# Kernel tuning notes

Hardware: AMD Instinct MI355X
Metric: run time of the kernel (lower is better)

Reference implementation:

```python
import jax, jax.numpy as jnp
import numpy as np

LAYERS = 10
EPS = 1e-08


def setup_inputs() -> dict:
    key = jax.random.key(0)
    # [B, agents, N, N] assignment logits; row 0 along dim 2 is the depot row
    output = jax.random.normal(key, (32, 8, 512, 512), dtype=jnp.float32)
    return {"output": output}


def reference(output):
    # Max-subtraction for numerical stability before exp.
    # Depot row: max over dim 3 only. Other rows: max over dims (1, 3).
    if LAYERS > 0:
        depots_max = jnp.max(output[:, :, :1, :], axis=3, keepdims=True)
        others_max = jnp.max(output[:, :, 1:, :], axis=(1, 3), keepdims=True)
        output = jnp.concatenate(
            [output[:, :, :1, :] - depots_max,
             output[:, :, 1:, :] - others_max],
            axis=2,
        )
    output = jnp.exp(output)
    # Sinkhorn-style alternating normalization; transpose(2,3) each iter
    # alternates which axis gets normalized.
    for _ in range(LAYERS):
        output = jnp.maximum(output, EPS)
        starts = output[:, :, :1, :]
        starts = starts / jnp.sum(starts, axis=3, keepdims=True)
        nexts = output[:, :, 1:, :]
        nexts = nexts / jnp.sum(nexts, axis=(1, 3), keepdims=True)
        output = jnp.concatenate([starts, nexts], axis=2)
        output = jnp.swapaxes(output, 2, 3)
    if LAYERS % 2 != 0:
        output = jnp.swapaxes(output, 2, 3)
    return output
```

## Files before the change

kernel.cpp:

```cpp
#include <hip/hip_runtime.h>
#include <hip/hip_cooperative_groups.h>
#include <math.h>

#define B 32
#define H 8
#define N 512
#define NBLK 256
#define TPB 512
#define RPB 64
#define OFF_E0   8388608
#define OFF_EC   (OFF_E0 + 131072)
#define OFF_PA   (OFF_EC + 131072)
#define OFF_PB   (OFF_PA + 131072)
#define OFF_C0A  (OFF_PB + 131072)
#define OFF_C0B  (OFF_C0A + 2048)

typedef float f32x4 __attribute__((ext_vector_type(4)));

__device__ __forceinline__ float atomLoad(const float* p) {
    return __hip_atomic_load(p, __ATOMIC_RELAXED, __HIP_MEMORY_SCOPE_AGENT);
}
__device__ __forceinline__ float2 atomLoad2(const float* p) {
    unsigned long long u = __hip_atomic_load(
        reinterpret_cast<const unsigned long long*>(p),
        __ATOMIC_RELAXED, __HIP_MEMORY_SCOPE_AGENT);
    union { unsigned long long u; float2 f; } cvt; cvt.u = u;
    return cvt.f;
}
__device__ __forceinline__ void atomStore(float* p, float v) {
    __hip_atomic_store(p, v, __ATOMIC_RELAXED, __HIP_MEMORY_SCOPE_AGENT);
}

__device__ __forceinline__ void group_barrier(int* cnt, int target) {
    __syncthreads();
    if (threadIdx.x == 0) {
        __hip_atomic_fetch_add(cnt, 1, __ATOMIC_RELAXED, __HIP_MEMORY_SCOPE_AGENT);
        while (__hip_atomic_load(cnt, __ATOMIC_RELAXED, __HIP_MEMORY_SCOPE_AGENT) < target)
            __builtin_amdgcn_s_sleep(1);
    }
    __syncthreads();
}

__global__ __launch_bounds__(128) void k_build(const float* __restrict__ in,
                                               float* __restrict__ G,
                                               float* __restrict__ E0,
                                               float* __restrict__ Ec,
                                               int* __restrict__ counters) {
    const int i = blockIdx.x;
    const int b = blockIdx.y;
    const int t = threadIdx.x;
    if (i == 0 && b == 0) {
#pragma unroll
        for (int k = 0; k < 4; ++k) counters[k * 128 + t] = 0;
    }
    const size_t inb = (size_t)b * H * N * N;
    float4 acc = make_float4(0.f, 0.f, 0.f, 0.f);
#pragma unroll
    for (int h = 0; h < H; ++h) {
        const float4 x = *reinterpret_cast<const float4*>(
            in + inb + ((size_t)h * N + i) * N + t * 4);
        float4 e;
        e.x = __expf(x.x); e.y = __expf(x.y); e.z = __expf(x.z); e.w = __expf(x.w);
        acc.x += e.x; acc.y += e.y; acc.z += e.z; acc.w += e.w;
        if (t == 0) Ec[(b * H + h) * N + i] = e.x;
        if (i == 0) *reinterpret_cast<float4*>(E0 + (b * H + h) * N + t * 4) = e;
    }
    *reinterpret_cast<float4*>(G + ((size_t)b * N + i) * N + t * 4) = acc;
}

__global__ __launch_bounds__(TPB) void k_coop(const float* __restrict__ G,
                                              const float* __restrict__ E0,
                                              const float* __restrict__ Ec,
                                              float* __restrict__ partA,
                                              float* __restrict__ partB,
                                              float* __restrict__ c0pA,
                                              float* __restrict__ c0pB,
                                              float* __restrict__ rv,
                                              float* __restrict__ r0v,
                                              float* __restrict__ cv,
                                              float* __restrict__ c0v,
                                              int* __restrict__ counters) {
    __shared__ float Gs[RPB][N];
    __shared__ float E0g[N];
    __shared__ float vec[N];
    __shared__ float EcS[H][RPB];
    __shared__ float rloc[RPB];
    __shared__ float c0rec[H];
    __shared__ float r0loc_s;

    const int blk = blockIdx.x;
    const int b = blk >> 3;
    const int g = blk & 7;
    const int rbase = g * RPB;
    const bool owner = (g == 0);
    const int tid = threadIdx.x;
    const int w = tid >> 6, lane = tid & 63;
    int* cnt = counters + b * 16;

    {
        const float4* Gg = reinterpret_cast<const float4*>(G + ((size_t)(b * N) + rbase) * N);
        float4* Gl = reinterpret_cast<float4*>(&Gs[0][0]);
#pragma unroll
        for (int k = 0; k < RPB * N / 4 / TPB; ++k) {
            const int t = k * TPB + tid;
            __builtin_amdgcn_global_load_lds(
                (const __attribute__((address_space(1))) void*)(Gg + t),
                (__attribute__((address_space(3))) void*)(Gl + t),
                16, 0, 0);
        }
    }
    EcS[tid >> 6][tid & 63] = Ec[(b * H + (tid >> 6)) * N + rbase + (tid & 63)];
    E0g[tid] = E0[(b * H + g) * N + tid];
    const float E00g = Ec[(b * H + g) * N];
    __syncthreads();

    for (int it = 0; it < 5; ++it) {
        if (it == 0) {
            vec[tid] = (tid == 0) ? 0.0f : 1.0f;
            if (tid < H) c0rec[tid] = 1.0f;
        } else {
            const float* pr = (it & 1) ? partB : partA;
            pr += ((size_t)b * N + tid) * 8;
            float cs = 0.0f;
#pragma unroll
            for (int k = 0; k < 4; ++k) {
                float2 d = atomLoad2(pr + 2 * k);
                cs += d.x + d.y;
            }
            vec[tid] = (tid == 0) ? 0.0f : 1.0f / cs;
            if (tid < H) {
                const float* qr = (it & 1) ? c0pB : c0pA;
                qr += (b * 8 + tid) * 8;
                float s = 0.0f;
#pragma unroll
                for (int k = 0; k < 4; ++k) {
                    float2 d = atomLoad2(qr + 2 * k);
                    s += d.x + d.y;
                }
                c0rec[tid] = 1.0f / s;
            }
        }
        __syncthreads();
        float cj[8];
#pragma unroll
        for (int k = 0; k < 8; ++k) cj[k] = vec[lane + 64 * k];
#pragma unroll
        for (int r8 = 0; r8 < 8; ++r8) {
            const int il = w * 8 + r8;
            float pacc = 0.0f;
#pragma unroll
            for (int k = 0; k < 8; ++k) pacc += Gs[il][lane + 64 * k] * cj[k];
#pragma unroll
            for (int s = 32; s > 0; s >>= 1) pacc += __shfl_down(pacc, s, 64);
            if (lane == 0) {
                float s2 = pacc;
#pragma unroll
                for (int h = 0; h < H; ++h) s2 += EcS[h][il] * c0rec[h];
                float rva = 1.0f / s2;
                rloc[il] = rva;
                if (it == 4) rv[b * N + rbase + il] = rva;
            }
        }
        if (w == g) {
            float pacc = 0.0f;
#pragma unroll
            for (int k = 0; k < 8; ++k) pacc += E0g[lane + 64 * k] * cj[k];
#pragma unroll
            for (int s = 32; s > 0; s >>= 1) pacc += __shfl_down(pacc, s, 64);
            if (lane == 0) {
                float v = 1.0f / (pacc + E00g * c0rec[g]);
                r0loc_s = v;
                if (it == 4) r0v[b * H + g] = v;
            }
        }
        __syncthreads();
        {
            float* pw = ((it + 1) & 1) ? partB : partA;
            float* qw = ((it + 1) & 1) ? c0pB : c0pA;
            const float r0l = r0loc_s;
            float acc = 0.0f;
            const int il0 = owner ? 1 : 0;
#pragma unroll 8
            for (int il = il0; il < RPB; ++il) acc += Gs[il][tid] * rloc[il];
            acc += E0g[tid] * r0l;
            atomStore(&pw[((size_t)b * N + tid) * 8 + g], acc);
            float q = EcS[w][lane] * ((owner && lane == 0) ? 0.0f : rloc[lane]);
            if (w == g && lane == 0) q += E00g * r0l;
#pragma unroll
            for (int s = 32; s > 0; s >>= 1) q += __shfl_down(q, s, 64);
            if (lane == 0) atomStore(&qw[(b * 8 + w) * 8 + g], q);
        }
        group_barrier(cnt, (it + 1) * 8);
    }
    if (owner) {
        const float* pr = partB + ((size_t)b * N + tid) * 8;
        float cs = 0.0f;
#pragma unroll
        for (int k = 0; k < 4; ++k) {
            float2 d = atomLoad2(pr + 2 * k);
            cs += d.x + d.y;
        }
        cv[b * N + tid] = (tid == 0) ? 1.0f : 1.0f / cs;
        if (tid < H) {
            const float* qr = c0pB + (b * 8 + tid) * 8;
            float s = 0.0f;
#pragma unroll
            for (int k = 0; k < 4; ++k) {
                float2 d = atomLoad2(qr + 2 * k);
                s += d.x + d.y;
            }
            c0v[b * H + tid] = 1.0f / s;
        }
    }
}

__global__ __launch_bounds__(256) void k_final(const float* __restrict__ in,
                                               const float* __restrict__ rv,
                                               const float* __restrict__ r0v,
                                               const float* __restrict__ cv,
                                               const float* __restrict__ c0v,
                                               float* __restrict__ out) {
    const size_t v0 = (size_t)blockIdx.x * 2048 + threadIdx.x;
    float4 x[8];
#pragma unroll
    for (int s = 0; s < 8; ++s)
        x[s] = reinterpret_cast<const float4*>(in)[v0 + (size_t)s * 256];
#pragma unroll
    for (int s = 0; s < 8; ++s) {
        const size_t v = v0 + (size_t)s * 256;
        const int j4 = (int)(v & 127);
        size_t rest = v >> 7;
        const int i = (int)(rest & 511); rest >>= 9;
        const int h = (int)(rest & 7);
        const int b = (int)(rest >> 3);
        const float R = (i == 0) ? r0v[b * H + h] : rv[b * N + i];
        float4 cl = reinterpret_cast<const float4*>(cv + b * N)[j4];
        if (j4 == 0) cl.x = c0v[b * H + h];
        f32x4 o;
        o.x = __expf(x[s].x) * R * cl.x;
        o.y = __expf(x[s].y) * R * cl.y;
        o.z = __expf(x[s].z) * R * cl.z;
        o.w = __expf(x[s].w) * R * cl.w;
        __builtin_nontemporal_store(o, reinterpret_cast<f32x4*>(out) + v);
    }
}

extern "C" void kernel_launch(void* const* d_in, const int* in_sizes, int n_in,
                              void* d_out, int out_size, void* d_ws, size_t ws_size,
                              hipStream_t stream) {
    (void)in_sizes; (void)n_in; (void)out_size; (void)ws_size;
    const float* in = (const float*)d_in[0];
    float* out = (float*)d_out;
    float* ws = (float*)d_ws;

    float* rv  = ws;
    float* cv  = ws + 16384;
    float* r0v = ws + 32768;
    float* c0v = ws + 33024;
    int* counters = (int*)(ws + 33280);

    float* G   = out;
    float* E0  = out + OFF_E0;
    float* Ec  = out + OFF_EC;
    float* pA  = out + OFF_PA;
    float* pB  = out + OFF_PB;
    float* c0A = out + OFF_C0A;
    float* c0B = out + OFF_C0B;

    k_build<<<dim3(N, B), 128, 0, stream>>>(in, G, E0, Ec, counters);

    void* args[] = {(void*)&G, (void*)&E0, (void*)&Ec, (void*)&pA, (void*)&pB,
                    (void*)&c0A, (void*)&c0B, (void*)&rv, (void*)&r0v,
                    (void*)&cv, (void*)&c0v, (void*)&counters};
    hipLaunchCooperativeKernel(reinterpret_cast<void*>(k_coop), dim3(NBLK), dim3(TPB),
                               args, 0, stream);

    k_final<<<8192, 256, 0, stream>>>(in, rv, r0v, cv, c0v, out);
}
```

Before: 196.4 us.

## Fuse exp/head-sum build stage into cooperative kernel, drop G round-trip

Removes the separate build kernel that computed exp of the input, summed it over heads into a global G matrix, and wrote E0/Ec side arrays. The cooperative kernel now reads the input directly, computes exponentials and head sums in registers, and writes them straight into shared memory. This avoids writing and re-reading the 32 MB G intermediate and one full kernel launch. The cost is that only 256 blocks read the 256 MB input, which may cap memory parallelism, and register pressure rises from the 16 float4 accumulators.

```diff
diff --git a/kernel.cpp b/kernel.cpp
--- a/kernel.cpp
+++ b/kernel.cpp
@@ -8,18 +8,13 @@
 #define NBLK 256
 #define TPB 512
 #define RPB 64
-#define OFF_E0   8388608
-#define OFF_EC   (OFF_E0 + 131072)
-#define OFF_PA   (OFF_EC + 131072)
+#define OFF_PA   8388608
 #define OFF_PB   (OFF_PA + 131072)
 #define OFF_C0A  (OFF_PB + 131072)
 #define OFF_C0B  (OFF_C0A + 2048)
 
 typedef float f32x4 __attribute__((ext_vector_type(4)));
 
-__device__ __forceinline__ float atomLoad(const float* p) {
-    return __hip_atomic_load(p, __ATOMIC_RELAXED, __HIP_MEMORY_SCOPE_AGENT);
-}
 __device__ __forceinline__ float2 atomLoad2(const float* p) {
     unsigned long long u = __hip_atomic_load(
         reinterpret_cast<const unsigned long long*>(p),
@@ -41,45 +36,20 @@
     __syncthreads();
 }
 
-__global__ __launch_bounds__(128) void k_build(const float* __restrict__ in,
-                                               float* __restrict__ G,
-                                               float* __restrict__ E0,
-                                               float* __restrict__ Ec,
-                                               int* __restrict__ counters) {
-    const int i = blockIdx.x;
-    const int b = blockIdx.y;
-    const int t = threadIdx.x;
-    if (i == 0 && b == 0) {
-#pragma unroll
-        for (int k = 0; k < 4; ++k) counters[k * 128 + t] = 0;
-    }
-    const size_t inb = (size_t)b * H * N * N;
-    float4 acc = make_float4(0.f, 0.f, 0.f, 0.f);
-#pragma unroll
-    for (int h = 0; h < H; ++h) {
-        const float4 x = *reinterpret_cast<const float4*>(
-            in + inb + ((size_t)h * N + i) * N + t * 4);
-        float4 e;
-        e.x = __expf(x.x); e.y = __expf(x.y); e.z = __expf(x.z); e.w = __expf(x.w);
-        acc.x += e.x; acc.y += e.y; acc.z += e.z; acc.w += e.w;
-        if (t == 0) Ec[(b * H + h) * N + i] = e.x;
-        if (i == 0) *reinterpret_cast<float4*>(E0 + (b * H + h) * N + t * 4) = e;
-    }
-    *reinterpret_cast<float4*>(G + ((size_t)b * N + i) * N + t * 4) = acc;
-}
-
-__global__ __launch_bounds__(TPB) void k_coop(const float* __restrict__ G,
-                                              const float* __restrict__ E0,
-                                              const float* __restrict__ Ec,
-                                              float* __restrict__ partA,
-                                              float* __restrict__ partB,
-                                              float* __restrict__ c0pA,
-                                              float* __restrict__ c0pB,
-                                              float* __restrict__ rv,
-                                              float* __restrict__ r0v,
-                                              float* __restrict__ cv,
-                                              float* __restrict__ c0v,
-                                              int* __restrict__ counters) {
+__global__ void k_zero(int* __restrict__ counters) {
+    counters[threadIdx.x] = 0;
+}
+
+__global__ __launch_bounds__(TPB, 2) void k_coopb(const float* __restrict__ in,
+                                                  float* __restrict__ partA,
+                                                  float* __restrict__ partB,
+                                                  float* __restrict__ c0pA,
+                                                  float* __restrict__ c0pB,
+                                                  float* __restrict__ rv,
+                                                  float* __restrict__ r0v,
+                                                  float* __restrict__ cv,
+                                                  float* __restrict__ c0v,
+                                                  int* __restrict__ counters) {
     __shared__ float Gs[RPB][N];
     __shared__ float E0g[N];
     __shared__ float vec[N];
@@ -97,22 +67,40 @@
     const int w = tid >> 6, lane = tid & 63;
     int* cnt = counters + b * 16;
 
-    {
-        const float4* Gg = reinterpret_cast<const float4*>(G + ((size_t)(b * N) + rbase) * N);
-        float4* Gl = reinterpret_cast<float4*>(&Gs[0][0]);
-#pragma unroll
-        for (int k = 0; k < RPB * N / 4 / TPB; ++k) {
-            const int t = k * TPB + tid;
-            __builtin_amdgcn_global_load_lds(
-                (const __attribute__((address_space(1))) void*)(Gg + t),
-                (__attribute__((address_space(3))) void*)(Gl + t),
-                16, 0, 0);
-        }
-    }
-    EcS[tid >> 6][tid & 63] = Ec[(b * H + (tid >> 6)) * N + rbase + (tid & 63)];
-    E0g[tid] = E0[(b * H + g) * N + tid];
-    const float E00g = Ec[(b * H + g) * N];
+    const int il4 = tid >> 7;
+    const int j4 = tid & 127;
+    const size_t inb = (size_t)b * H * N * N;
+    float4 acc[16];
+#pragma unroll
+    for (int c = 0; c < 16; ++c) acc[c] = make_float4(0.f, 0.f, 0.f, 0.f);
+#pragma unroll
+    for (int h = 0; h < H; ++h) {
+        const float* base = in + inb + (size_t)h * N * N + (size_t)rbase * N;
+        float4 xv[16];
+#pragma unroll
+        for (int c = 0; c < 16; ++c)
+            xv[c] = *reinterpret_cast<const float4*>(base + (size_t)(c * 4 + il4) * N + j4 * 4);
+#pragma unroll
+        for (int c = 0; c < 16; ++c) {
+            float4 e;
+            e.x = __expf(xv[c].x); e.y = __expf(xv[c].y);
+            e.z = __expf(xv[c].z); e.w = __expf(xv[c].w);
+            acc[c].x += e.x; acc[c].y += e.y; acc[c].z += e.z; acc[c].w += e.w;
+            if (j4 == 0) EcS[h][c * 4 + il4] = e.x;
+        }
+    }
+#pragma unroll
+    for (int c = 0; c < 16; ++c)
+        *reinterpret_cast<float4*>(&Gs[c * 4 + il4][j4 * 4]) = acc[c];
+    if (tid < 128) {
+        const float4 xr = *reinterpret_cast<const float4*>(in + inb + (size_t)g * N * N + tid * 4);
+        E0g[tid * 4 + 0] = __expf(xr.x);
+        E0g[tid * 4 + 1] = __expf(xr.y);
+        E0g[tid * 4 + 2] = __expf(xr.z);
+        E0g[tid * 4 + 3] = __expf(xr.w);
+    }
     __syncthreads();
+    const float E00g = E0g[0];
 
     for (int it = 0; it < 5; ++it) {
         if (it == 0) {
@@ -178,12 +166,12 @@
             float* pw = ((it + 1) & 1) ? partB : partA;
             float* qw = ((it + 1) & 1) ? c0pB : c0pA;
             const float r0l = r0loc_s;
-            float acc = 0.0f;
+            float acc2 = 0.0f;
             const int il0 = owner ? 1 : 0;
 #pragma unroll 8
-            for (int il = il0; il < RPB; ++il) acc += Gs[il][tid] * rloc[il];
-            acc += E0g[tid] * r0l;
-            atomStore(&pw[((size_t)b * N + tid) * 8 + g], acc);
+            for (int il = il0; il < RPB; ++il) acc2 += Gs[il][tid] * rloc[il];
+            acc2 += E0g[tid] * r0l;
+            atomStore(&pw[((size_t)b * N + tid) * 8 + g], acc2);
             float q = EcS[w][lane] * ((owner && lane == 0) ? 0.0f : rloc[lane]);
             if (w == g && lane == 0) q += E00g * r0l;
 #pragma unroll
@@ -259,20 +247,16 @@
     float* c0v = ws + 33024;
     int* counters = (int*)(ws + 33280);
 
-    float* G   = out;
-    float* E0  = out + OFF_E0;
-    float* Ec  = out + OFF_EC;
     float* pA  = out + OFF_PA;
     float* pB  = out + OFF_PB;
     float* c0A = out + OFF_C0A;
     float* c0B = out + OFF_C0B;
 
-    k_build<<<dim3(N, B), 128, 0, stream>>>(in, G, E0, Ec, counters);
-
-    void* args[] = {(void*)&G, (void*)&E0, (void*)&Ec, (void*)&pA, (void*)&pB,
-                    (void*)&c0A, (void*)&c0B, (void*)&rv, (void*)&r0v,
-                    (void*)&cv, (void*)&c0v, (void*)&counters};
-    hipLaunchCooperativeKernel(reinterpret_cast<void*>(k_coop), dim3(NBLK), dim3(TPB),
+    k_zero<<<1, 512, 0, stream>>>(counters);
+
+    void* args[] = {(void*)&in, (void*)&pA, (void*)&pB, (void*)&c0A, (void*)&c0B,
+                    (void*)&rv, (void*)&r0v, (void*)&cv, (void*)&c0v, (void*)&counters};
+    hipLaunchCooperativeKernel(reinterpret_cast<void*>(k_coopb), dim3(NBLK), dim3(TPB),
                                args, 0, stream);
 
     k_final<<<8192, 256, 0, stream>>>(in, rv, r0v, cv, c0v, out);
```

After: 336.3 us. 1.71x slower.
